# Performance work log

Hardware: AMD Instinct MI355X
Metric: run time of the kernel (lower is better)

The kernel has to match this reference:

```python
import jax, jax.numpy as jnp
import numpy as np

K = 3          # kernel_size
PAD = 1        # padding
HEADS = 4
C = 128
K2 = K * K


def setup_inputs() -> dict:
    key = jax.random.key(0)
    k1, k2, k3, k4 = jax.random.split(key, 4)
    B, H, W = 4, 128, 128
    x = jax.random.normal(k1, (B, H, W, C), jnp.float32)
    w_qkv = jax.random.normal(k2, (K2 * K2 * HEADS, C), jnp.float32) * 0.02
    w_v = jax.random.normal(k3, (K2, C, C), jnp.float32) * np.sqrt(2.0 / (K2 * C))
    w_proj = jax.random.normal(k4, (C, C), jnp.float32) * 0.02
    return {"x": x, "w_qkv": w_qkv, "w_v": w_v, "w_proj": w_proj}


def _csa(x, w_qkv, w_v, w_proj):
    B, H, W, Cc = x.shape
    hd = Cc // HEADS
    scale = hd ** (-0.5)
    N = H * W
    # attention map: Linear(C -> k^4*heads); pool is identity for stride=1
    att = jnp.einsum('bhwc,oc->bhwo', x, w_qkv)                      # [B,H,W,81*heads]
    att = att.reshape(B, N, HEADS, K2, K2).transpose(0, 2, 1, 3, 4)  # [B,heads,N,k2,k2]
    att = jax.nn.softmax(att * scale, axis=-1)
    # unfold x into per-location 3x3 windows (patch index p = di*K + dj)
    xp = jnp.pad(x, ((0, 0), (PAD, PAD), (PAD, PAD), (0, 0)))
    patches = jnp.stack([xp[:, di:di + H, dj:dj + W, :]
                         for di in range(K) for dj in range(K)], axis=3)  # [B,H,W,k2,C]
    v = patches.reshape(B, N, K2, Cc)
    # grouped 1x1 conv == per-window-position CxC matmul
    v = jnp.einsum('pij,bnpj->bnpi', w_v, v)                          # [B,N,k2,C]
    v = v.reshape(B, N, K2, HEADS, hd).transpose(0, 3, 1, 2, 4)       # [B,heads,N,k2,hd]
    out = jnp.einsum('bhnpq,bhnqd->bhnpd', att, v)                    # [B,heads,N,k2,hd]
    # -> [B, C, k2, H, W] with channel index = head*hd + d (matches torch fold layout)
    out = out.transpose(0, 1, 4, 3, 2).reshape(B, Cc, K2, H, W)
    # fold: scatter-add overlapping patches back to (H, W)
    acc = jnp.zeros((B, Cc, H + 2 * PAD, W + 2 * PAD), x.dtype)
    p = 0
    for di in range(K):
        for dj in range(K):
            acc = acc.at[:, :, di:di + H, dj:dj + W].add(out[:, :, p])
            p += 1
    y = acc[:, :, PAD:PAD + H, PAD:PAD + W].transpose(0, 2, 3, 1)     # [B,H,W,C]
    return jnp.einsum('bhwc,oc->bhwo', y, w_proj)


def reference(x, w_qkv, w_v, w_proj):
    return _csa(x, w_qkv, w_v, w_proj)
```

## Files before the change

kernel.cpp:

```cpp
#include <hip/hip_runtime.h>


typedef short bf16x8 __attribute__((ext_vector_type(8)));
typedef float f32x4  __attribute__((ext_vector_type(4)));
typedef float v2f    __attribute__((ext_vector_type(2)));

#define SCALE 0.17677669529663687f

__device__ __forceinline__ unsigned short f2bf(float f) {
  unsigned u = __float_as_uint(f);
  u = (u + 0x7fffu + ((u >> 16) & 1u)) >> 16;
  return (unsigned short)u;
}
__device__ __forceinline__ float bf2f(unsigned short s) {
  return __uint_as_float(((unsigned)s) << 16);
}
__device__ __forceinline__ unsigned pk2bf(float lo, float hi) {
  unsigned a = __float_as_uint(lo) + 0x8000u;
  unsigned b = __float_as_uint(hi) + 0x8000u;
  return __builtin_amdgcn_perm(b, a, 0x07060302u);
}
__device__ __forceinline__ bf16x8 ld16(const unsigned short* p) {
  union { bf16x8 v; uint4 u; } r;
  r.u = *(const uint4*)p;
  return r.v;
}

__global__ __launch_bounds__(256) void cvt_kernel(const float* __restrict__ wq,
                                                  const float* __restrict__ wv,
                                                  const float* __restrict__ wp,
                                                  unsigned short* __restrict__ wqb,
                                                  unsigned short* __restrict__ wvb2,
                                                  unsigned short* __restrict__ wpb2) {
  int i = blockIdx.x * 256 + threadIdx.x;
  if (i >= 30848) return;
  if (i < 10368) {
    long off = (long)i * 4;
    float4 v = *(const float4*)(wq + off);
    ushort4 o;
    o.x = f2bf(v.x); o.y = f2bf(v.y); o.z = f2bf(v.z); o.w = f2bf(v.w);
    *(ushort4*)(wqb + off) = o;
    return;
  }
  const float* s;
  unsigned short* d;
  if (i < 28800) {
    int it = i - 10368;
    int l = it & 63, mk = it >> 6;
    int kk = mk & 3, m = (mk >> 2) & 1, qcg = mk >> 3;
    int cg = qcg & 3, q = qcg >> 2;
    int chan = cg * 32 + m * 16 + (l & 15);
    int k0 = kk * 32 + (l >> 4) * 8;
    s = wv + (long)q * 16384 + chan * 128 + k0;
    d = wvb2 + (long)it * 8;
  } else {
    int it = i - 28800;
    int l = it & 63, kk = (it >> 6) & 3, tn = it >> 8;
    int col = tn * 16 + (l & 15);
    int k0 = kk * 32 + (l >> 4) * 8;
    s = wp + (long)col * 128 + k0;
    d = wpb2 + (long)it * 8;
  }
  float4 a = *(const float4*)s, b = *(const float4*)(s + 4);
  ushort4 o0, o1;
  o0.x = f2bf(a.x); o0.y = f2bf(a.y); o0.z = f2bf(a.z); o0.w = f2bf(a.w);
  o1.x = f2bf(b.x); o1.y = f2bf(b.y); o1.z = f2bf(b.z); o1.w = f2bf(b.w);
  *(ushort4*)d = o0;
  *(ushort4*)(d + 4) = o1;
}

__device__ __forceinline__ void softmax9(const float* L, unsigned short* attile,
                                         int row, int p) {
  float mx = L[0];
#pragma unroll
  for (int q = 1; q < 9; q++) mx = fmaxf(mx, L[q]);
  float e[9], s = 0.f;
#pragma unroll
  for (int q = 0; q < 9; q++) { e[q] = __expf((L[q] - mx) * SCALE); s += e[q]; }
  float inv = 1.f / s;
#pragma unroll
  for (int q = 0; q < 9; q++) attile[row * 90 + q * 10 + p] = f2bf(e[q] * inv);
}

__global__ __launch_bounds__(512, 4) void att_kernel(const float* __restrict__ x,
                                                     const unsigned short* __restrict__ wqb,
                                                     unsigned* __restrict__ attb) {
  __shared__ unsigned short A[64 * 136];
  __shared__ unsigned short Bl[96 * 136];
  __shared__ float lg[64][84];
  const int t = threadIdx.x;
  const long m0 = (long)blockIdx.x * 64;
#pragma unroll
  for (int k = 0; k < 4; k++) {
    int i = t + k * 512;
    int row = i >> 5, seg = i & 31;
    float4 v = *(const float4*)(x + (m0 + row) * 128 + seg * 4);
    *(uint2*)((unsigned*)A + row * 68 + seg * 2) =
        make_uint2(pk2bf(v.x, v.y), pk2bf(v.z, v.w));
  }
  const int w = t >> 6, lane = t & 63, qd = lane >> 4, l15 = lane & 15;
  const int rw = w & 3, th = w >> 2;
  const int sr0 = t / 9, sp0 = t - sr0 * 9;
  const int sr1 = (t + 512) / 9, sp1 = (t + 512) - sr1 * 9;
  int dsto[6], srco[6];
#pragma unroll
  for (int k = 0; k < 6; k++) {
    int i = t + k * 512;
    if (i < 2880) {
      int q = i / 320, rem = i - q * 320, n = rem / 5, j = rem - n * 5;
      dsto[k] = (int)(((size_t)(q * 4) * 65536 + m0 + n) * 5 + j);
      srco[k] = n * 45 + q * 5 + j;
    } else { dsto[k] = -1; srco[k] = 0; }
  }
  __syncthreads();
  bf16x8 af[4];
#pragma unroll
  for (int kk = 0; kk < 4; kk++)
    af[kk] = ld16(A + (rw * 16 + l15) * 136 + kk * 32 + qd * 8);

  unsigned short* attile = Bl;
  for (int h = 0; h < 4; h++) {
    __syncthreads();
#pragma unroll
    for (int k = 0; k < 3; k++) {
      int i = t + k * 512;
      if (i < 1296) {
        int row = i >> 4, seg = i & 15;
        const uint4 v = *(const uint4*)(wqb + (long)(h * 81 + row) * 128 + seg * 8);
        *(uint4*)((unsigned*)Bl + row * 68 + seg * 4) = v;
      }
    }
    __syncthreads();
    f32x4 acc[3] = {};
#pragma unroll
    for (int kk = 0; kk < 4; kk++)
#pragma unroll
      for (int tn = 0; tn < 3; tn++) {
        bf16x8 bf = ld16(Bl + ((th * 3 + tn) * 16 + l15) * 136 + kk * 32 + qd * 8);
        acc[tn] = __builtin_amdgcn_mfma_f32_16x16x32_bf16(af[kk], bf, acc[tn], 0, 0, 0);
      }
#pragma unroll
    for (int tn = 0; tn < 3; tn++)
#pragma unroll
      for (int r = 0; r < 4; r++) {
        int col = (th * 3 + tn) * 16 + l15;
        if (col < 81) lg[rw * 16 + qd * 4 + r][col] = acc[tn][r];
      }
    __syncthreads();
    softmax9(&lg[sr0][sp0 * 9], attile, sr0, sp0);
    if (t < 64) softmax9(&lg[sr1][sp1 * 9], attile, sr1, sp1);
    __syncthreads();
#pragma unroll
    for (int k = 0; k < 6; k++)
      if (dsto[k] >= 0)
        attb[dsto[k] + h * 327680] = ((const unsigned*)attile)[srco[k]];
  }
}

__global__ __launch_bounds__(512, 4) void av_kernel(const float* __restrict__ x,
                                                    const unsigned short* __restrict__ wvb2,
                                                    const unsigned* __restrict__ attb,
                                                    const unsigned short* __restrict__ wpb2,
                                                    float* __restrict__ out) {
  __shared__ unsigned short A[144 * 136];
  __shared__ unsigned short S[100 * 136];
  __shared__ unsigned aLs[2400];
  const int t = threadIdx.x;
  const int bb = blockIdx.z;
  const int r0 = blockIdx.y * 8, c0 = blockIdx.x * 8;
  const int l15 = t & 15, qd = (t >> 4) & 3, wvi = t >> 6;
  const int lane = t & 63;
  const int cg = wvi & 3, lp = wvi >> 2;
  const int n = (wvi & 3) * 16 + l15, lr = n >> 3, lc = n & 7;
  const int g = (wvi >> 2) * 4 + qd, head = g >> 1;
  const long nb = (long)bb * 16384;
  unsigned* Sdw = (unsigned*)S;
  unsigned* Adw = (unsigned*)A;

  int xbI[4];
#pragma unroll
  for (int i = 0; i < 4; i++) {
    int tile = lp * 4 + i;
    int ml = tile < 7 ? tile * 16 + l15 : 0;
    xbI[i] = (ml / 10) * 12 + (ml % 10) + 13;
  }

#pragma unroll
  for (int k = 0; k < 9; k++) {
    int i = t + k * 512;
    int row = i >> 5, seg = i & 31;
    int gr = r0 - 2 + row / 12, gc = c0 - 2 + row % 12;
    float4 v = make_float4(0.f, 0.f, 0.f, 0.f);
    if (gr >= 0 && gr < 128 && gc >= 0 && gc < 128)
      v = *(const float4*)(x + (nb + gr * 128 + gc) * 128 + seg * 4);
    *(uint2*)(Adw + row * 68 + seg * 2) = make_uint2(pk2bf(v.x, v.y), pk2bf(v.z, v.w));
  }

  int aoff[4], aidx[4];
#pragma unroll
  for (int k = 0; k < 4; k++) {
    int i = t + k * 512;
    if (i < 2000) {
      int hh = i / 500, rem = i - hh * 500, row = rem / 5, j5 = rem - row * 5;
      int gr = r0 - 1 + row / 10, gc = c0 - 1 + row % 10;
      aidx[k] = hh * 600 + row * 6 + j5;
      aoff[k] = (gr >= 0 && gr < 128 && gc >= 0 && gc < 128)
                    ? (int)(((size_t)hh * 65536 + nb + gr * 128 + gc) * 5 + j5)
                    : -1;
    } else { aidx[k] = -1; aoff[k] = -1; }
  }
  const unsigned short* pwv = wvb2 + cg * 4096 + lane * 8;

  v2f y2[8];
#pragma unroll
  for (int i = 0; i < 8; i++) y2[i] = (v2f){0.f, 0.f};

  unsigned avv[4];
  bf16x8 wvf[2][4];

#define LOAD_A(qq)                                                              \
  { _Pragma("unroll") for (int k = 0; k < 4; k++)                               \
      avv[k] = (aoff[k] >= 0) ? attb[aoff[k] + (qq) * 1310720] : 0u; }
#define LOAD_WV(qq)                                                             \
  { _Pragma("unroll") for (int m = 0; m < 2; m++)                               \
    _Pragma("unroll") for (int kk = 0; kk < 4; kk++)                            \
      wvf[m][kk] = *(const bf16x8*)(pwv + (size_t)(qq) * 16384 +                \
                                    (m * 4 + kk) * 512); }

  LOAD_A(0)
  LOAD_WV(0)

  for (int q = 0; q < 9; q++) {
    const int qoff = (q / 3) * 12 + (q % 3) - 13;
    __syncthreads();

#pragma unroll
    for (int k = 0; k < 4; k++)
      if (aidx[k] >= 0) aLs[aidx[k]] = avv[k];

#pragma unroll
    for (int i = 0; i < 4; i++) {
      const int tile = lp * 4 + i;
      if (tile < 7) {
        int xr = xbI[i] + qoff;
        xr = xr > 143 ? 143 : xr;
        bf16x8 bx[4];
#pragma unroll
        for (int kk = 0; kk < 4; kk++)
          bx[kk] = ld16(A + xr * 136 + kk * 32 + qd * 8);
        f32x4 acc[2];
#pragma unroll
        for (int m = 0; m < 2; m++) acc[m] = (f32x4){0.f, 0.f, 0.f, 0.f};
#pragma unroll
        for (int kk = 0; kk < 4; kk++)
#pragma unroll
          for (int m = 0; m < 2; m++)
            acc[m] = __builtin_amdgcn_mfma_f32_16x16x32_bf16(wvf[m][kk], bx[kk],
                                                             acc[m], 0, 0, 0);
        int loc = tile * 16 + l15;
        if (loc < 100) {
#pragma unroll
          for (int m = 0; m < 2; m++)
            *(uint2*)(Sdw + loc * 68 + cg * 16 + m * 8 + qd * 2) =
                make_uint2(pk2bf(acc[m][0], acc[m][1]),
                           pk2bf(acc[m][2], acc[m][3]));
        }
      }
    }
    __syncthreads();
    if (q < 8) { LOAD_A(q + 1) LOAD_WV(q + 1) }

    const unsigned short* aS = (const unsigned short*)aLs;
    const int mlb = lr * 10 + lc + 11;
#pragma unroll
    for (int p = 0; p < 9; p++) {
      const int ml = mlb + (1 - p / 3) * 10 + (1 - p % 3);
      const float a = bf2f(aS[head * 1200 + ml * 12 + p]);
      const v2f a2 = {a, a};
      const uint4* Sr = (const uint4*)(Sdw + ml * 68 + g * 8);
#pragma unroll
      for (int v4 = 0; v4 < 2; v4++) {
        const uint4 u = Sr[v4];
        v2f xv;
        const int yi = v4 * 4;
        xv.x = __uint_as_float(u.x << 16); xv.y = __uint_as_float(u.x & 0xffff0000u);
        y2[yi + 0] += a2 * xv;
        xv.x = __uint_as_float(u.y << 16); xv.y = __uint_as_float(u.y & 0xffff0000u);
        y2[yi + 1] += a2 * xv;
        xv.x = __uint_as_float(u.z << 16); xv.y = __uint_as_float(u.z & 0xffff0000u);
        y2[yi + 2] += a2 * xv;
        xv.x = __uint_as_float(u.w << 16); xv.y = __uint_as_float(u.w & 0xffff0000u);
        y2[yi + 3] += a2 * xv;
      }
    }
  }

  __syncthreads();
  unsigned short* yb = A;
  {
    uint4 pk[2];
#pragma unroll
    for (int v4 = 0; v4 < 2; v4++) {
      pk[v4].x = pk2bf(y2[v4 * 4 + 0].x, y2[v4 * 4 + 0].y);
      pk[v4].y = pk2bf(y2[v4 * 4 + 1].x, y2[v4 * 4 + 1].y);
      pk[v4].z = pk2bf(y2[v4 * 4 + 2].x, y2[v4 * 4 + 2].y);
      pk[v4].w = pk2bf(y2[v4 * 4 + 3].x, y2[v4 * 4 + 3].y);
    }
    uint4* dst = (uint4*)(Adw + n * 68 + g * 8);
    dst[0] = pk[0]; dst[1] = pk[1];
  }
  __syncthreads();
  f32x4 pacc[4] = {};
#pragma unroll
  for (int kk = 0; kk < 4; kk++) {
    bf16x8 afr = ld16(yb + ((wvi & 3) * 16 + l15) * 136 + kk * 32 + qd * 8);
#pragma unroll
    for (int tn = 0; tn < 4; tn++) {
      bf16x8 bfr = *(const bf16x8*)(wpb2 + (((wvi >> 2) * 4 + tn) * 4 + kk) * 512 +
                                    lane * 8);
      pacc[tn] = __builtin_amdgcn_mfma_f32_16x16x32_bf16(afr, bfr, pacc[tn], 0, 0, 0);
    }
  }
#pragma unroll
  for (int tn = 0; tn < 4; tn++)
#pragma unroll
    for (int r = 0; r < 4; r++) {
      int nl = (wvi & 3) * 16 + qd * 4 + r;
      int col = ((wvi >> 2) * 4 + tn) * 16 + l15;
      out[(nb + (r0 + (nl >> 3)) * 128 + (c0 + (nl & 7))) * 128 + col] = pacc[tn][r];
    }
}

extern "C" void kernel_launch(void* const* d_in, const int* in_sizes, int n_in,
                              void* d_out, int out_size, void* d_ws, size_t ws_size,
                              hipStream_t stream) {
  const float* x  = (const float*)d_in[0];
  const float* wq = (const float*)d_in[1];
  const float* wv = (const float*)d_in[2];
  const float* wp = (const float*)d_in[3];
  char* w = (char*)d_ws;
  unsigned*       attb = (unsigned*)w;
  unsigned short* wqb  = (unsigned short*)(w + 47185920);
  unsigned short* wvb2 = wqb + 41472;
  unsigned short* wpb2 = wvb2 + 147456;

  cvt_kernel<<<121, 256, 0, stream>>>(wq, wv, wp, wqb, wvb2, wpb2);
  att_kernel<<<1024, 512, 0, stream>>>(x, wqb, attb);
  dim3 g3(16, 16, 4);
  av_kernel<<<g3, 512, 0, stream>>>(x, wvb2, attb, wpb2, (float*)d_out);
}
```

Baseline: 190.4 us.

## Pre-swizzle w_qkv into MFMA fragment layout and double-buffer attention tile stores

The cvt kernel now writes w_qkv in a per-lane MFMA B-fragment layout, zero-padded to 96 columns per head. The att kernel can then load B fragments straight from global/L2 instead of staging each head's weights through shared memory. The softmax output tile is double-buffered, and each head's global store is deferred to the next iteration, which removes two barriers per head. Less LDS lets launch bounds rise to 6 blocks per CU, at the cost of repeated global weight reads per wave.

```diff
diff --git a/kernel.cpp b/kernel.cpp
--- a/kernel.cpp
+++ b/kernel.cpp
@@ -29,23 +29,33 @@
 __global__ __launch_bounds__(256) void cvt_kernel(const float* __restrict__ wq,
                                                   const float* __restrict__ wv,
                                                   const float* __restrict__ wp,
-                                                  unsigned short* __restrict__ wqb,
+                                                  unsigned short* __restrict__ wqb2,
                                                   unsigned short* __restrict__ wvb2,
                                                   unsigned short* __restrict__ wpb2) {
   int i = blockIdx.x * 256 + threadIdx.x;
-  if (i >= 30848) return;
-  if (i < 10368) {
-    long off = (long)i * 4;
-    float4 v = *(const float4*)(wq + off);
-    ushort4 o;
-    o.x = f2bf(v.x); o.y = f2bf(v.y); o.z = f2bf(v.z); o.w = f2bf(v.w);
-    *(ushort4*)(wqb + off) = o;
+  if (i >= 26624) return;
+  if (i < 6144) {
+    int l = i & 63, rest = i >> 6;
+    int kk = rest & 3, r2 = rest >> 2;
+    int tile = r2 % 6, h = r2 / 6;
+    int col = tile * 16 + (l & 15);
+    int k0 = kk * 32 + (l >> 4) * 8;
+    unsigned short* d = wqb2 + (long)i * 8;
+    ushort4 o0 = make_ushort4(0, 0, 0, 0), o1 = make_ushort4(0, 0, 0, 0);
+    if (col < 81) {
+      const float* s = wq + (long)(h * 81 + col) * 128 + k0;
+      float4 a = *(const float4*)s, b = *(const float4*)(s + 4);
+      o0.x = f2bf(a.x); o0.y = f2bf(a.y); o0.z = f2bf(a.z); o0.w = f2bf(a.w);
+      o1.x = f2bf(b.x); o1.y = f2bf(b.y); o1.z = f2bf(b.z); o1.w = f2bf(b.w);
+    }
+    *(ushort4*)d = o0;
+    *(ushort4*)(d + 4) = o1;
     return;
   }
   const float* s;
   unsigned short* d;
-  if (i < 28800) {
-    int it = i - 10368;
+  if (i < 24576) {
+    int it = i - 6144;
     int l = it & 63, mk = it >> 6;
     int kk = mk & 3, m = (mk >> 2) & 1, qcg = mk >> 3;
     int cg = qcg & 3, q = qcg >> 2;
@@ -54,7 +64,7 @@
     s = wv + (long)q * 16384 + chan * 128 + k0;
     d = wvb2 + (long)it * 8;
   } else {
-    int it = i - 28800;
+    int it = i - 24576;
     int l = it & 63, kk = (it >> 6) & 3, tn = it >> 8;
     int col = tn * 16 + (l & 15);
     int k0 = kk * 32 + (l >> 4) * 8;
@@ -82,11 +92,10 @@
   for (int q = 0; q < 9; q++) attile[row * 90 + q * 10 + p] = f2bf(e[q] * inv);
 }
 
-__global__ __launch_bounds__(512, 4) void att_kernel(const float* __restrict__ x,
-                                                     const unsigned short* __restrict__ wqb,
+__global__ __launch_bounds__(512, 6) void att_kernel(const float* __restrict__ x,
+                                                     const unsigned short* __restrict__ wqb2,
                                                      unsigned* __restrict__ attb) {
-  __shared__ unsigned short A[64 * 136];
-  __shared__ unsigned short Bl[96 * 136];
+  __shared__ unsigned short AT[11520];
   __shared__ float lg[64][84];
   const int t = threadIdx.x;
   const long m0 = (long)blockIdx.x * 64;
@@ -95,50 +104,42 @@
     int i = t + k * 512;
     int row = i >> 5, seg = i & 31;
     float4 v = *(const float4*)(x + (m0 + row) * 128 + seg * 4);
-    *(uint2*)((unsigned*)A + row * 68 + seg * 2) =
+    *(uint2*)((unsigned*)AT + row * 68 + seg * 2) =
         make_uint2(pk2bf(v.x, v.y), pk2bf(v.z, v.w));
   }
   const int w = t >> 6, lane = t & 63, qd = lane >> 4, l15 = lane & 15;
   const int rw = w & 3, th = w >> 2;
   const int sr0 = t / 9, sp0 = t - sr0 * 9;
   const int sr1 = (t + 512) / 9, sp1 = (t + 512) - sr1 * 9;
-  int dsto[6], srco[6];
-#pragma unroll
-  for (int k = 0; k < 6; k++) {
-    int i = t + k * 512;
-    if (i < 2880) {
-      int q = i / 320, rem = i - q * 320, n = rem / 5, j = rem - n * 5;
-      dsto[k] = (int)(((size_t)(q * 4) * 65536 + m0 + n) * 5 + j);
-      srco[k] = n * 45 + q * 5 + j;
-    } else { dsto[k] = -1; srco[k] = 0; }
-  }
   __syncthreads();
   bf16x8 af[4];
 #pragma unroll
   for (int kk = 0; kk < 4; kk++)
-    af[kk] = ld16(A + (rw * 16 + l15) * 136 + kk * 32 + qd * 8);
-
-  unsigned short* attile = Bl;
+    af[kk] = ld16(AT + (rw * 16 + l15) * 136 + kk * 32 + qd * 8);
+  const unsigned short* pwb = wqb2 + lane * 8;
+  unsigned* ATdw = (unsigned*)AT;
+
+#define STORE_ATT(hh)                                                           \
+  { const unsigned* sb = ATdw + ((hh)&1) * 2880;                                \
+    _Pragma("unroll") for (int k = 0; k < 6; k++) {                             \
+      int i = t + k * 512;                                                      \
+      if (i < 2880) {                                                           \
+        int q = i / 320, rem = i - q * 320, n = rem / 5, j = rem - n * 5;       \
+        attb[((size_t)(q * 4 + (hh)) * 65536 + m0 + n) * 5 + j] =               \
+            sb[n * 45 + q * 5 + j];                                             \
+      }                                                                         \
+    } }
+
   for (int h = 0; h < 4; h++) {
-    __syncthreads();
-#pragma unroll
-    for (int k = 0; k < 3; k++) {
-      int i = t + k * 512;
-      if (i < 1296) {
-        int row = i >> 4, seg = i & 15;
-        const uint4 v = *(const uint4*)(wqb + (long)(h * 81 + row) * 128 + seg * 8);
-        *(uint4*)((unsigned*)Bl + row * 68 + seg * 4) = v;
-      }
-    }
-    __syncthreads();
     f32x4 acc[3] = {};
 #pragma unroll
     for (int kk = 0; kk < 4; kk++)
 #pragma unroll
       for (int tn = 0; tn < 3; tn++) {
-        bf16x8 bf = ld16(Bl + ((th * 3 + tn) * 16 + l15) * 136 + kk * 32 + qd * 8);
+        bf16x8 bf = *(const bf16x8*)(pwb + ((h * 6 + th * 3 + tn) * 4 + kk) * 512);
         acc[tn] = __builtin_amdgcn_mfma_f32_16x16x32_bf16(af[kk], bf, acc[tn], 0, 0, 0);
       }
+    __syncthreads();
 #pragma unroll
     for (int tn = 0; tn < 3; tn++)
 #pragma unroll
@@ -147,14 +148,13 @@
         if (col < 81) lg[rw * 16 + qd * 4 + r][col] = acc[tn][r];
       }
     __syncthreads();
+    if (h > 0) STORE_ATT(h - 1)
+    unsigned short* attile = AT + (h & 1) * 5760;
     softmax9(&lg[sr0][sp0 * 9], attile, sr0, sp0);
     if (t < 64) softmax9(&lg[sr1][sp1 * 9], attile, sr1, sp1);
-    __syncthreads();
-#pragma unroll
-    for (int k = 0; k < 6; k++)
-      if (dsto[k] >= 0)
-        attb[dsto[k] + h * 327680] = ((const unsigned*)attile)[srco[k]];
-  }
+  }
+  __syncthreads();
+  STORE_ATT(3)
 }
 
 __global__ __launch_bounds__(512, 4) void av_kernel(const float* __restrict__ x,
@@ -340,12 +340,12 @@
   const float* wp = (const float*)d_in[3];
   char* w = (char*)d_ws;
   unsigned*       attb = (unsigned*)w;
-  unsigned short* wqb  = (unsigned short*)(w + 47185920);
-  unsigned short* wvb2 = wqb + 41472;
+  unsigned short* wqb2 = (unsigned short*)(w + 47185920);
+  unsigned short* wvb2 = wqb2 + 49152;
   unsigned short* wpb2 = wvb2 + 147456;
 
-  cvt_kernel<<<121, 256, 0, stream>>>(wq, wv, wp, wqb, wvb2, wpb2);
-  att_kernel<<<1024, 512, 0, stream>>>(x, wqb, attb);
+  cvt_kernel<<<104, 256, 0, stream>>>(wq, wv, wp, wqb2, wvb2, wpb2);
+  att_kernel<<<1024, 512, 0, stream>>>(x, wqb2, attb);
   dim3 g3(16, 16, 4);
   av_kernel<<<g3, 512, 0, stream>>>(x, wvb2, attb, wpb2, (float*)d_out);
 }
```

Measured after the change: 208.7 us. 1.1x slower.
